# Kernel tuning notes

Measured on AMD Instinct MI355X. Metric: run time of the kernel, lower is better.

The kernel has to match this reference:

```python
import jax, jax.numpy as jnp
import numpy as np

U, G, I, D = 10000, 3000, 8000, 32
LAYERS, SOCIAL_LAYERS = 3, 2
NNZ_UI, NNZ_GI = 720000, 440000
L_MEM = 20
B = 4096


def setup_inputs() -> dict:
    key = jax.random.key(0)
    ks = jax.random.split(key, 24)
    s_u = 1.0 / np.sqrt(U).astype(np.float32)
    s_i = 1.0 / np.sqrt(I).astype(np.float32)
    return {
        "group_inputs": jax.random.randint(ks[0], (B,), 0, G, dtype=jnp.int32),
        "item_inputs": jax.random.randint(ks[1], (B,), 0, I, dtype=jnp.int32),
        "user_emb": jax.random.normal(ks[2], (U, D), jnp.float32) * 0.1,
        "group_emb": jax.random.normal(ks[3], (G, D), jnp.float32) * 0.1,
        "item_emb": jax.random.normal(ks[4], (I, D), jnp.float32) * 0.1,
        "ui_rows": jax.random.randint(ks[5], (NNZ_UI,), 0, U + I, dtype=jnp.int32),
        "ui_cols": jax.random.randint(ks[6], (NNZ_UI,), 0, U + I, dtype=jnp.int32),
        "ui_vals": jax.random.uniform(ks[7], (NNZ_UI,), jnp.float32) * 0.02,
        "gi_rows": jax.random.randint(ks[8], (NNZ_GI,), 0, G + I, dtype=jnp.int32),
        "gi_cols": jax.random.randint(ks[9], (NNZ_GI,), 0, G + I, dtype=jnp.int32),
        "gi_vals": jax.random.uniform(ks[10], (NNZ_GI,), jnp.float32) * 0.02,
        "overlap_user": jax.random.normal(ks[11], (U, U), jnp.float32) * (0.1 * s_u),
        "overlap_item": jax.random.normal(ks[12], (I, I), jnp.float32) * (0.1 * s_i),
        "all_group_users": jax.random.randint(ks[13], (G, L_MEM), 0, U, dtype=jnp.int32),
        "all_group_mask": jax.random.uniform(ks[14], (G, L_MEM), jnp.float32) / L_MEM,
        "gate_w1": jax.random.normal(ks[15], (D, D), jnp.float32) * 0.1,
        "gate_b1": jnp.zeros((D,), jnp.float32),
        "gate_w2": jax.random.normal(ks[16], (D, 1), jnp.float32) * 0.1,
        "gate_b2": jnp.zeros((1,), jnp.float32),
        "pred_w1": jax.random.normal(ks[17], (D, 8), jnp.float32) * 0.1,
        "pred_b1": jnp.zeros((8,), jnp.float32),
        "pred_w2": jax.random.normal(ks[18], (8, 1), jnp.float32) * 0.1,
        "pred_b2": jnp.zeros((1,), jnp.float32),
    }


def _spmm(rows, cols, vals, x, n):
    # COO sparse-dense matmul: out[r] += vals * x[c]
    return jax.ops.segment_sum(vals[:, None] * x[cols], rows, num_segments=n)


def reference(group_inputs, item_inputs, user_emb, group_emb, item_emb,
              ui_rows, ui_cols, ui_vals, gi_rows, gi_cols, gi_vals,
              overlap_user, overlap_item, all_group_users, all_group_mask,
              gate_w1, gate_b1, gate_w2, gate_b2,
              pred_w1, pred_b1, pred_w2, pred_b2):
    # ---- GraphConvolution: user-item propagation ----
    ui = jnp.concatenate([user_emb, item_emb])           # [U+I, D]
    embs_ui = [ui]
    for _ in range(LAYERS):
        ui = _spmm(ui_rows, ui_cols, ui_vals, ui, U + I)
        embs_ui.append(ui)
    user_layers = [e[:U] for e in embs_ui]
    item_layers = [e[U:] for e in embs_ui]
    user_emb_for_user = jnp.mean(jnp.stack(user_layers, 1), axis=1)   # [U, D]
    item_emb_for_user = jnp.mean(jnp.stack(item_layers, 1), axis=1)   # [I, D]

    # ---- group-item propagation ----
    gi = jnp.concatenate([group_emb, item_emb_for_user])  # [G+I, D]
    embs_gi = [gi]
    for _ in range(LAYERS):
        gi = _spmm(gi_rows, gi_cols, gi_vals, gi, G + I)
        embs_gi.append(gi)
    group_gi = [e[:G] for e in embs_gi]
    item_gi = [e[G:] for e in embs_gi]
    i_emb = jnp.mean(jnp.stack(item_gi, 1), axis=1)       # [I, D]

    g_layers = []
    for i in range(LAYERS + 1):
        if i % 2 == 0:
            g_layers.append(group_gi[i])
        else:
            emb_in = jnp.concatenate([group_emb, item_layers[i - 1]])
            g_layers.append(_spmm(gi_rows, gi_cols, gi_vals, emb_in, G + I)[:G])
    g_emb = jnp.mean(jnp.stack(g_layers, 1), axis=1)      # [G, D]

    # ---- SocialRelationshipAgg (dense power-series + gathered pooling) ----
    ue = user_emb_for_user
    acc = ue
    for _ in range(SOCIAL_LAYERS):
        ue = overlap_user @ ue
        acc = acc + ue
    members = acc[all_group_users]                        # [G, L, D]
    group_userlayer = jnp.einsum('gl,gld->gd', all_group_mask, members)

    # ---- Gate ----
    x = jnp.concatenate([g_emb, group_userlayer])         # [2G, D]
    h = jax.nn.relu(x @ gate_w1 + gate_b1)
    w = jax.nn.sigmoid(h @ gate_w2 + gate_b2)             # [2G, 1]
    group_final = w[:G] * g_emb + w[G:] * group_userlayer

    # ---- OverlapGraphConvolution on items ----
    it = i_emb
    iacc = it
    for _ in range(SOCIAL_LAYERS):
        it = overlap_item @ it
        iacc = iacc + it

    # ---- Predict ----
    ge = group_final[group_inputs]                        # [B, D]
    ie = iacc[item_inputs]                                # [B, D]
    p = jax.nn.relu((ge * ie) @ pred_w1 + pred_b1)
    return jax.nn.sigmoid(p @ pred_w2 + pred_b2)          # [B, 1]
```

## Files before the change

### kernel.cpp

```cpp
#include <hip/hip_runtime.h>
#include <math.h>

#define U_N 10000
#define G_N 3000
#define I_N 8000
#define D_N 32
#define NNZ_UI 720000
#define NNZ_GI 440000
#define L_MEM 20
#define B_N 4096
#define UI_N (U_N + I_N)
#define GI_N (G_N + I_N)
#define CAP 128

static __host__ int cdiv(int a, int b) { return (a + b - 1) / b; }

typedef __attribute__((ext_vector_type(8))) short bf16x8;
typedef __attribute__((ext_vector_type(4))) float f32x4;

__device__ __forceinline__ short f32_to_bf16(float f) {
    unsigned u = __float_as_uint(f);
    unsigned r = (u + 0x7FFFu + ((u >> 16) & 1u)) >> 16;
    return (short)r;
}


__global__ __launch_bounds__(256) void bucket_fill2(const int* __restrict__ uir,
                                                    const int* __restrict__ uic,
                                                    const float* __restrict__ uiv,
                                                    const int* __restrict__ gir,
                                                    const int* __restrict__ gic,
                                                    const float* __restrict__ giv,
                                                    int* __restrict__ cnt_ui,
                                                    int* __restrict__ cnt_gi,
                                                    int2* __restrict__ bkt_ui,
                                                    int2* __restrict__ bkt_gi) {
    int i = blockIdx.x * 256 + threadIdx.x;
    if (i < NNZ_UI) {
        int r = uir[i];
        int pos = atomicAdd(&cnt_ui[r], 1);
        if (pos < CAP) {
            int2 e; e.x = uic[i]; e.y = __float_as_int(uiv[i]);
            bkt_ui[(size_t)r * CAP + pos] = e;
        }
        return;
    }
    int k = i - NNZ_UI;
    if (k < NNZ_GI) {
        int r = gir[k];
        int pos = atomicAdd(&cnt_gi[r], 1);
        if (pos < CAP) {
            int2 e; e.x = gic[k]; e.y = __float_as_int(giv[k]);
            bkt_gi[(size_t)r * CAP + pos] = e;
        }
    }
}

#define GATHER(e) ((e.x < split) ? x1[(size_t)e.x * 32 + d] \
                                 : x2[(size_t)(e.x - split) * 32 + d])

__global__ __launch_bounds__(256) void spmm_split(const int* __restrict__ cnt,
                                                  const int2* __restrict__ bkt,
                                                  const float* __restrict__ x1,
                                                  const float* __restrict__ x2,
                                                  int split,
                                                  float* __restrict__ out, int nrows) {
    int row = blockIdx.x * 8 + (threadIdx.x >> 5);
    if (row >= nrows) return;
    int d = threadIdx.x & 31;
    int deg = cnt[row];
    if (deg > CAP) deg = CAP;
    const int2* bk = bkt + (size_t)row * CAP;
    float acc = 0.f;
    int j = 0;
    for (; j + 3 < deg; j += 4) {
        int2 e0 = bk[j], e1 = bk[j + 1], e2 = bk[j + 2], e3 = bk[j + 3];
        float g0 = GATHER(e0), g1 = GATHER(e1), g2 = GATHER(e2), g3 = GATHER(e3);
        acc = fmaf(__int_as_float(e0.y), g0, acc);
        acc = fmaf(__int_as_float(e1.y), g1, acc);
        acc = fmaf(__int_as_float(e2.y), g2, acc);
        acc = fmaf(__int_as_float(e3.y), g3, acc);
    }
    for (; j < deg; ++j) {
        int2 e = bk[j];
        acc = fmaf(__int_as_float(e.y), GATHER(e), acc);
    }
    out[(size_t)row * 32 + d] = acc;
}

__global__ __launch_bounds__(256) void spmm_g2(const int* __restrict__ cnt,
                                               const int2* __restrict__ bkt,
                                               const float* __restrict__ gemb0,
                                               const float* __restrict__ iemb0,
                                               const float* __restrict__ ui2item,
                                               float* __restrict__ gt1,
                                               float* __restrict__ gt3) {
    int row = blockIdx.x * 8 + (threadIdx.x >> 5);
    if (row >= 2 * G_N) return;
    int g = (row < G_N) ? row : row - G_N;
    const float* x1 = gemb0;
    const float* x2 = (row < G_N) ? iemb0 : ui2item;
    const int split = G_N;
    float* out = (row < G_N) ? gt1 : gt3;
    int d = threadIdx.x & 31;
    int deg = cnt[g];
    if (deg > CAP) deg = CAP;
    const int2* bk = bkt + (size_t)g * CAP;
    float acc = 0.f;
    int j = 0;
    for (; j + 3 < deg; j += 4) {
        int2 e0 = bk[j], e1 = bk[j + 1], e2 = bk[j + 2], e3 = bk[j + 3];
        float g0 = GATHER(e0), g1 = GATHER(e1), g2 = GATHER(e2), g3 = GATHER(e3);
        acc = fmaf(__int_as_float(e0.y), g0, acc);
        acc = fmaf(__int_as_float(e1.y), g1, acc);
        acc = fmaf(__int_as_float(e2.y), g2, acc);
        acc = fmaf(__int_as_float(e3.y), g3, acc);
    }
    for (; j < deg; ++j) {
        int2 e = bk[j];
        acc = fmaf(__int_as_float(e.y), GATHER(e), acc);
    }
    out[(size_t)g * 32 + d] = acc;
}
#undef GATHER


__global__ __launch_bounds__(256) void mean_ui(const float* __restrict__ uemb,
                                               const float* __restrict__ iemb0,
                                               const float* __restrict__ ui1,
                                               const float* __restrict__ ui2,
                                               const float* __restrict__ ui3,
                                               float* __restrict__ uefu,
                                               float* __restrict__ accu,
                                               float* __restrict__ iefu) {
    int idx = blockIdx.x * 256 + threadIdx.x;
    if (idx >= UI_N * 32) return;
    const int UOFF = U_N * 32;
    float base = (idx < UOFF) ? uemb[idx] : iemb0[idx - UOFF];
    float m = 0.25f * (base + ui1[idx] + ui2[idx] + ui3[idx]);
    if (idx < UOFF) { uefu[idx] = m; accu[idx] = m; }
    else iefu[idx - UOFF] = m;
}

__global__ __launch_bounds__(256) void mean_gi_items(const float* __restrict__ iefu,
                                                     const float* __restrict__ gi1,
                                                     const float* __restrict__ gi2,
                                                     const float* __restrict__ gi3,
                                                     float* __restrict__ iemb,
                                                     float* __restrict__ iacc) {
    int idx = blockIdx.x * 256 + threadIdx.x;
    if (idx >= I_N * 32) return;
    const int GOFF = G_N * 32;
    float m = 0.25f * (iefu[idx] + gi1[GOFF + idx] + gi2[GOFF + idx] + gi3[GOFF + idx]);
    iemb[idx] = m;
    iacc[idx] = m;
}


__global__ __launch_bounds__(256) void pack_xb(const float* __restrict__ x,
                                               short* __restrict__ XB, int N, int ktiles) {
    int idx = blockIdx.x * 256 + threadIdx.x;
    int total = ktiles * 2 * 64;
    if (idx >= total) return;
    int lane = idx & 63;
    int th = idx >> 6;
    int h = th & 1;
    int t = th >> 1;
    int q = lane >> 4;
    int n = (lane & 15) + h * 16;
    short v[8];
#pragma unroll
    for (int j = 0; j < 8; ++j) {
        int c = t * 32 + q * 8 + j;
        v[j] = (c < N) ? f32_to_bf16(x[(size_t)c * 32 + n]) : (short)0;
    }
    short* dst = XB + (size_t)idx * 8;
#pragma unroll
    for (int j = 0; j < 8; ++j) dst[j] = v[j];
}

__global__ __launch_bounds__(512) void dense_mfma_b(const float* __restrict__ A,
                                                    const short* __restrict__ XB,
                                                    float* __restrict__ out,
                                                    const float* __restrict__ add1,
                                                    int N, int ktiles) {
    __shared__ float red[8 * 512];
    int tid = threadIdx.x;
    int w = tid >> 6;
    int lane = tid & 63;
    int r0 = blockIdx.x << 4;
    int m = lane & 15;
    int q = lane >> 4;
    const float* arow = A + (size_t)(r0 + m) * N + q * 8;
    const bf16x8* xb = (const bf16x8*)XB;
    f32x4 acc0 = {0.f, 0.f, 0.f, 0.f};
    f32x4 acc1 = {0.f, 0.f, 0.f, 0.f};
    for (int t = w; t < ktiles; t += 8) {
        int c0 = t * 32;
        bf16x8 afrag;
        if (c0 + 32 <= N) {
            float4 lo = *(const float4*)(arow + c0);
            float4 hi = *(const float4*)(arow + c0 + 4);
            afrag[0] = f32_to_bf16(lo.x); afrag[1] = f32_to_bf16(lo.y);
            afrag[2] = f32_to_bf16(lo.z); afrag[3] = f32_to_bf16(lo.w);
            afrag[4] = f32_to_bf16(hi.x); afrag[5] = f32_to_bf16(hi.y);
            afrag[6] = f32_to_bf16(hi.z); afrag[7] = f32_to_bf16(hi.w);
        } else {
#pragma unroll
            for (int j = 0; j < 8; ++j) {
                int c = c0 + q * 8 + j;
                afrag[j] = (c < N) ? f32_to_bf16(arow[c0 + j]) : (short)0;
            }
        }
        bf16x8 b0 = xb[(size_t)(t * 2 + 0) * 64 + lane];
        bf16x8 b1 = xb[(size_t)(t * 2 + 1) * 64 + lane];
        acc0 = __builtin_amdgcn_mfma_f32_16x16x32_bf16(afrag, b0, acc0, 0, 0, 0);
        acc1 = __builtin_amdgcn_mfma_f32_16x16x32_bf16(afrag, b1, acc1, 0, 0, 0);
    }
    float* my = red + w * 512;
#pragma unroll
    for (int i = 0; i < 4; ++i) {
        my[(q * 4 + i) * 32 + m]      = acc0[i];
        my[(q * 4 + i) * 32 + m + 16] = acc1[i];
    }
    __syncthreads();
    float s = red[tid];
#pragma unroll
    for (int wv = 1; wv < 8; ++wv) s += red[wv * 512 + tid];
    int row = tid >> 5;
    int col = tid & 31;
    size_t o = (size_t)(r0 + row) * 32 + col;
    out[o] = add1 ? (out[o] + add1[o] + s) : s;
}

__global__ __launch_bounds__(256) void pool_gate_mix(const int* __restrict__ users,
                                                     const float* __restrict__ mask,
                                                     const float* __restrict__ accu,
                                                     const float* __restrict__ gemb0,
                                                     const float* __restrict__ gt1,
                                                     const float* __restrict__ gi2,
                                                     const float* __restrict__ gt3,
                                                     const float* __restrict__ W1,
                                                     const float* __restrict__ b1,
                                                     const float* __restrict__ w2,
                                                     const float* __restrict__ b2,
                                                     float* __restrict__ gfin) {
    int g = blockIdx.x * 8 + (threadIdx.x >> 5);
    if (g >= G_N) return;
    int j = threadIdx.x & 31;
    size_t gj = (size_t)g * 32 + j;
    float ge = 0.25f * (gemb0[gj] + gt1[gj] + gi2[gj] + gt3[gj]);
    float gl = 0.f;
#pragma unroll
    for (int l = 0; l < L_MEM; ++l) {
        int u = users[g * L_MEM + l];
        gl = fmaf(mask[g * L_MEM + l], accu[(size_t)u * 32 + j], gl);
    }
    float h1 = b1[j], h2 = b1[j];
#pragma unroll
    for (int k = 0; k < 32; ++k) {
        float w = W1[k * 32 + j];
        h1 = fmaf(__shfl(ge, k, 32), w, h1);
        h2 = fmaf(__shfl(gl, k, 32), w, h2);
    }
    float w2j = w2[j];
    float t1 = fmaxf(h1, 0.f) * w2j;
    float t2 = fmaxf(h2, 0.f) * w2j;
#pragma unroll
    for (int off = 16; off >= 1; off >>= 1) {
        t1 += __shfl_xor(t1, off, 32);
        t2 += __shfl_xor(t2, off, 32);
    }
    float bb = b2[0];
    float wa = 1.f / (1.f + expf(-(t1 + bb)));
    float wb = 1.f / (1.f + expf(-(t2 + bb)));
    gfin[gj] = wa * ge + wb * gl;
}

__global__ __launch_bounds__(256) void predict_kernel(const int* __restrict__ gidx,
                                                      const int* __restrict__ iidx,
                                                      const float* __restrict__ gfin,
                                                      const float* __restrict__ iacc,
                                                      const float* __restrict__ pw1,
                                                      const float* __restrict__ pb1,
                                                      const float* __restrict__ pw2,
                                                      const float* __restrict__ pb2,
                                                      float* __restrict__ out) {
    int b = blockIdx.x * 256 + threadIdx.x;
    if (b >= B_N) return;
    const float* ge = gfin + (size_t)gidx[b] * 32;
    const float* ie = iacc + (size_t)iidx[b] * 32;
    float p[8];
#pragma unroll
    for (int j = 0; j < 8; ++j) p[j] = pb1[j];
    for (int d = 0; d < 32; ++d) {
        float t = ge[d] * ie[d];
#pragma unroll
        for (int j = 0; j < 8; ++j) p[j] = fmaf(t, pw1[d * 8 + j], p[j]);
    }
    float s = pb2[0];
#pragma unroll
    for (int j = 0; j < 8; ++j) s = fmaf(fmaxf(p[j], 0.f), pw2[j], s);
    out[b] = 1.f / (1.f + expf(-s));
}


extern "C" void kernel_launch(void* const* d_in, const int* in_sizes, int n_in,
                              void* d_out, int out_size, void* d_ws, size_t ws_size,
                              hipStream_t stream) {
    const int*   gin   = (const int*)d_in[0];
    const int*   iin   = (const int*)d_in[1];
    const float* uemb  = (const float*)d_in[2];
    const float* gemb0 = (const float*)d_in[3];
    const float* iemb0 = (const float*)d_in[4];
    const int*   uir   = (const int*)d_in[5];
    const int*   uic   = (const int*)d_in[6];
    const float* uiv   = (const float*)d_in[7];
    const int*   gir   = (const int*)d_in[8];
    const int*   gic   = (const int*)d_in[9];
    const float* giv   = (const float*)d_in[10];
    const float* ov_u  = (const float*)d_in[11];
    const float* ov_i  = (const float*)d_in[12];
    const int*   agu   = (const int*)d_in[13];
    const float* agm   = (const float*)d_in[14];
    const float* gw1   = (const float*)d_in[15];
    const float* gb1   = (const float*)d_in[16];
    const float* gw2   = (const float*)d_in[17];
    const float* gb2   = (const float*)d_in[18];
    const float* pw1   = (const float*)d_in[19];
    const float* pb1   = (const float*)d_in[20];
    const float* pw2   = (const float*)d_in[21];
    const float* pb2   = (const float*)d_in[22];
    float* out = (float*)d_out;

    const int KT_U = (U_N + 31) / 32;
    const int KT_I = I_N / 32;

    char* wp = (char*)d_ws;
    auto alloc = [&](size_t nbytes) -> void* {
        void* p = (void*)wp;
        wp += (nbytes + 255) & ~(size_t)255;
        return p;
    };
    int*   cnt_ui = (int*)alloc((size_t)UI_N * 4);
    int*   cnt_gi = (int*)alloc((size_t)GI_N * 4);
    size_t zbytes = (size_t)(wp - (char*)cnt_ui);

    int2*  bkt_ui = (int2*)alloc((size_t)UI_N * CAP * 8);
    int2*  bkt_gi = (int2*)alloc((size_t)GI_N * CAP * 8);
    float* uea  = (float*)alloc((size_t)U_N * 32 * 4);
    float* ita  = (float*)alloc((size_t)I_N * 32 * 4);
    float* ui1  = (float*)alloc((size_t)UI_N * 32 * 4);
    float* ui2  = (float*)alloc((size_t)UI_N * 32 * 4);
    float* ui3  = (float*)alloc((size_t)UI_N * 32 * 4);
    float* gi1  = (float*)alloc((size_t)GI_N * 32 * 4);
    float* gi2  = (float*)alloc((size_t)GI_N * 32 * 4);
    float* gi3  = (float*)alloc((size_t)GI_N * 32 * 4);
    float* uefu = (float*)alloc((size_t)U_N * 32 * 4);
    float* iefu = (float*)alloc((size_t)I_N * 32 * 4);
    float* iemb = (float*)alloc((size_t)I_N * 32 * 4);
    float* gt1  = (float*)alloc((size_t)G_N * 32 * 4);
    float* gt3  = (float*)alloc((size_t)G_N * 32 * 4);
    float* accu = (float*)alloc((size_t)U_N * 32 * 4);
    float* gfin = (float*)alloc((size_t)G_N * 32 * 4);
    float* iacc = (float*)alloc((size_t)I_N * 32 * 4);
    short* xbu  = (short*)alloc((size_t)KT_U * 2 * 64 * 8 * 2);
    short* xbi  = (short*)alloc((size_t)KT_I * 2 * 64 * 8 * 2);

    (void)hipMemsetAsync(cnt_ui, 0, zbytes, stream);
    bucket_fill2<<<cdiv(NNZ_UI + NNZ_GI, 256), 256, 0, stream>>>(
        uir, uic, uiv, gir, gic, giv, cnt_ui, cnt_gi, bkt_ui, bkt_gi);

    spmm_split<<<cdiv(UI_N, 8), 256, 0, stream>>>(cnt_ui, bkt_ui, uemb, iemb0, U_N, ui1, UI_N);
    spmm_split<<<cdiv(UI_N, 8), 256, 0, stream>>>(cnt_ui, bkt_ui, ui1, ui1 + (size_t)U_N * 32, U_N, ui2, UI_N);
    spmm_split<<<cdiv(UI_N, 8), 256, 0, stream>>>(cnt_ui, bkt_ui, ui2, ui2 + (size_t)U_N * 32, U_N, ui3, UI_N);
    spmm_g2<<<cdiv(2 * G_N, 8), 256, 0, stream>>>(cnt_gi, bkt_gi, gemb0, iemb0,
                                                  ui2 + (size_t)U_N * 32, gt1, gt3);
    mean_ui<<<cdiv(UI_N * 32, 256), 256, 0, stream>>>(uemb, iemb0, ui1, ui2, ui3, uefu, accu, iefu);

    spmm_split<<<cdiv(GI_N, 8), 256, 0, stream>>>(cnt_gi, bkt_gi, gemb0, iefu, G_N, gi1, GI_N);
    spmm_split<<<cdiv(GI_N, 8), 256, 0, stream>>>(cnt_gi, bkt_gi, gi1, gi1 + (size_t)G_N * 32, G_N, gi2, GI_N);
    spmm_split<<<cdiv(GI_N, 8), 256, 0, stream>>>(cnt_gi, bkt_gi, gi2, gi2 + (size_t)G_N * 32, G_N, gi3, GI_N);
    mean_gi_items<<<cdiv(I_N * 32, 256), 256, 0, stream>>>(iefu, gi1, gi2, gi3, iemb, iacc);

    const int U_STRIPS = U_N / 16, I_STRIPS = I_N / 16;
    pack_xb<<<cdiv(KT_U * 128, 256), 256, 0, stream>>>(uefu, xbu, U_N, KT_U);
    dense_mfma_b<<<U_STRIPS, 512, 0, stream>>>(ov_u, xbu, uea, nullptr, U_N, KT_U);
    pack_xb<<<cdiv(KT_U * 128, 256), 256, 0, stream>>>(uea, xbu, U_N, KT_U);
    dense_mfma_b<<<U_STRIPS, 512, 0, stream>>>(ov_u, xbu, accu, uea, U_N, KT_U);

    pool_gate_mix<<<cdiv(G_N, 8), 256, 0, stream>>>(agu, agm, accu, gemb0, gt1, gi2, gt3,
                                                    gw1, gb1, gw2, gb2, gfin);

    pack_xb<<<cdiv(KT_I * 128, 256), 256, 0, stream>>>(iemb, xbi, I_N, KT_I);
    dense_mfma_b<<<I_STRIPS, 512, 0, stream>>>(ov_i, xbi, ita, nullptr, I_N, KT_I);
    pack_xb<<<cdiv(KT_I * 128, 256), 256, 0, stream>>>(ita, xbi, I_N, KT_I);
    dense_mfma_b<<<I_STRIPS, 512, 0, stream>>>(ov_i, xbi, iacc, ita, I_N, KT_I);

    predict_kernel<<<cdiv(B_N, 256), 256, 0, stream>>>(gin, iin, gfin, iacc,
                                                       pw1, pb1, pw2, pb2, out);
}
```

Baseline: 1.106 ms.

## Compute final item overlap layer only for queried items and trim GI spmm

Marks the unique item indices used by the prediction batch and builds a compact row list. The last dense overlap-item matmul now runs only over those rows, instead of all 8000, reading only the needed rows of the large overlap matrix. The third group-item spmm layer skips group rows, whose results are not consumed. It adds a small marking kernel and an atomic-built row list. Rows of iacc for unqueried items are left incomplete.

```diff
diff --git a/kernel.cpp b/kernel.cpp
--- a/kernel.cpp
+++ b/kernel.cpp
@@ -56,6 +56,20 @@
     }
 }
 
+__global__ __launch_bounds__(256) void mark_items(const int* __restrict__ iidx,
+                                                  int* __restrict__ iflags,
+                                                  int* __restrict__ icount,
+                                                  int* __restrict__ ilist) {
+    int b = blockIdx.x * 256 + threadIdx.x;
+    if (b >= B_N) return;
+    int it = iidx[b];
+    if (it < 0 || it >= I_N) return;
+    if (atomicExch(&iflags[it], 1) == 0) {
+        int p = atomicAdd(icount, 1);
+        if (p < B_N) ilist[p] = it;
+    }
+}
+
 #define GATHER(e) ((e.x < split) ? x1[(size_t)e.x * 32 + d] \
                                  : x2[(size_t)(e.x - split) * 32 + d])
 
@@ -64,8 +78,9 @@
                                                   const float* __restrict__ x1,
                                                   const float* __restrict__ x2,
                                                   int split,
-                                                  float* __restrict__ out, int nrows) {
-    int row = blockIdx.x * 8 + (threadIdx.x >> 5);
+                                                  float* __restrict__ out,
+                                                  int row0, int nrows) {
+    int row = row0 + blockIdx.x * 8 + (threadIdx.x >> 5);
     if (row >= nrows) return;
     int d = threadIdx.x & 31;
     int deg = cnt[row];
@@ -233,6 +248,68 @@
     out[o] = add1 ? (out[o] + add1[o] + s) : s;
 }
 
+__global__ __launch_bounds__(512) void dense_mfma_trim(const float* __restrict__ A,
+                                                       const short* __restrict__ XB,
+                                                       float* __restrict__ out,
+                                                       const float* __restrict__ add1,
+                                                       const int* __restrict__ rowlist,
+                                                       const int* __restrict__ rowcount,
+                                                       int N, int ktiles) {
+    __shared__ float red[8 * 512];
+    int cnt = *rowcount;
+    if (cnt < 1) return;
+    if (cnt > B_N) cnt = B_N;
+    int r0 = blockIdx.x << 4;
+    if (r0 >= cnt) return;
+    int tid = threadIdx.x;
+    int w = tid >> 6;
+    int lane = tid & 63;
+    int m = lane & 15;
+    int q = lane >> 4;
+    int ci = r0 + m;
+    if (ci >= cnt) ci = cnt - 1;
+    int arow_g = rowlist[ci];
+    if (arow_g < 0 || arow_g >= I_N) arow_g = 0;
+    const float* arow = A + (size_t)arow_g * N + q * 8;
+    const bf16x8* xb = (const bf16x8*)XB;
+    f32x4 acc0 = {0.f, 0.f, 0.f, 0.f};
+    f32x4 acc1 = {0.f, 0.f, 0.f, 0.f};
+    for (int t = w; t < ktiles; t += 8) {
+        int c0 = t * 32;
+        float4 lo = *(const float4*)(arow + c0);
+        float4 hi = *(const float4*)(arow + c0 + 4);
+        bf16x8 afrag;
+        afrag[0] = f32_to_bf16(lo.x); afrag[1] = f32_to_bf16(lo.y);
+        afrag[2] = f32_to_bf16(lo.z); afrag[3] = f32_to_bf16(lo.w);
+        afrag[4] = f32_to_bf16(hi.x); afrag[5] = f32_to_bf16(hi.y);
+        afrag[6] = f32_to_bf16(hi.z); afrag[7] = f32_to_bf16(hi.w);
+        bf16x8 b0 = xb[(size_t)(t * 2 + 0) * 64 + lane];
+        bf16x8 b1 = xb[(size_t)(t * 2 + 1) * 64 + lane];
+        acc0 = __builtin_amdgcn_mfma_f32_16x16x32_bf16(afrag, b0, acc0, 0, 0, 0);
+        acc1 = __builtin_amdgcn_mfma_f32_16x16x32_bf16(afrag, b1, acc1, 0, 0, 0);
+    }
+    float* my = red + w * 512;
+#pragma unroll
+    for (int i = 0; i < 4; ++i) {
+        my[(q * 4 + i) * 32 + m]      = acc0[i];
+        my[(q * 4 + i) * 32 + m + 16] = acc1[i];
+    }
+    __syncthreads();
+    float s = red[tid];
+#pragma unroll
+    for (int wv = 1; wv < 8; ++wv) s += red[wv * 512 + tid];
+    int row = tid >> 5;
+    int col = tid & 31;
+    int gidx = r0 + row;
+    if (gidx < cnt) {
+        int orow = rowlist[gidx];
+        if (orow >= 0 && orow < I_N) {
+            size_t o = (size_t)orow * 32 + col;
+            out[o] = out[o] + add1[o] + s;
+        }
+    }
+}
+
 __global__ __launch_bounds__(256) void pool_gate_mix(const int* __restrict__ users,
                                                      const float* __restrict__ mask,
                                                      const float* __restrict__ accu,
@@ -344,7 +421,10 @@
     };
     int*   cnt_ui = (int*)alloc((size_t)UI_N * 4);
     int*   cnt_gi = (int*)alloc((size_t)GI_N * 4);
+    int*   iflags = (int*)alloc((size_t)I_N * 4);
+    int*   icount = (int*)alloc(4);
     size_t zbytes = (size_t)(wp - (char*)cnt_ui);
+    int*   ilist  = (int*)alloc((size_t)B_N * 4);
 
     int2*  bkt_ui = (int2*)alloc((size_t)UI_N * CAP * 8);
     int2*  bkt_gi = (int2*)alloc((size_t)GI_N * CAP * 8);
@@ -370,17 +450,18 @@
     (void)hipMemsetAsync(cnt_ui, 0, zbytes, stream);
     bucket_fill2<<<cdiv(NNZ_UI + NNZ_GI, 256), 256, 0, stream>>>(
         uir, uic, uiv, gir, gic, giv, cnt_ui, cnt_gi, bkt_ui, bkt_gi);
-
-    spmm_split<<<cdiv(UI_N, 8), 256, 0, stream>>>(cnt_ui, bkt_ui, uemb, iemb0, U_N, ui1, UI_N);
-    spmm_split<<<cdiv(UI_N, 8), 256, 0, stream>>>(cnt_ui, bkt_ui, ui1, ui1 + (size_t)U_N * 32, U_N, ui2, UI_N);
-    spmm_split<<<cdiv(UI_N, 8), 256, 0, stream>>>(cnt_ui, bkt_ui, ui2, ui2 + (size_t)U_N * 32, U_N, ui3, UI_N);
+    mark_items<<<cdiv(B_N, 256), 256, 0, stream>>>(iin, iflags, icount, ilist);
+
+    spmm_split<<<cdiv(UI_N, 8), 256, 0, stream>>>(cnt_ui, bkt_ui, uemb, iemb0, U_N, ui1, 0, UI_N);
+    spmm_split<<<cdiv(UI_N, 8), 256, 0, stream>>>(cnt_ui, bkt_ui, ui1, ui1 + (size_t)U_N * 32, U_N, ui2, 0, UI_N);
+    spmm_split<<<cdiv(UI_N, 8), 256, 0, stream>>>(cnt_ui, bkt_ui, ui2, ui2 + (size_t)U_N * 32, U_N, ui3, 0, UI_N);
     spmm_g2<<<cdiv(2 * G_N, 8), 256, 0, stream>>>(cnt_gi, bkt_gi, gemb0, iemb0,
                                                   ui2 + (size_t)U_N * 32, gt1, gt3);
     mean_ui<<<cdiv(UI_N * 32, 256), 256, 0, stream>>>(uemb, iemb0, ui1, ui2, ui3, uefu, accu, iefu);
 
-    spmm_split<<<cdiv(GI_N, 8), 256, 0, stream>>>(cnt_gi, bkt_gi, gemb0, iefu, G_N, gi1, GI_N);
-    spmm_split<<<cdiv(GI_N, 8), 256, 0, stream>>>(cnt_gi, bkt_gi, gi1, gi1 + (size_t)G_N * 32, G_N, gi2, GI_N);
-    spmm_split<<<cdiv(GI_N, 8), 256, 0, stream>>>(cnt_gi, bkt_gi, gi2, gi2 + (size_t)G_N * 32, G_N, gi3, GI_N);
+    spmm_split<<<cdiv(GI_N, 8), 256, 0, stream>>>(cnt_gi, bkt_gi, gemb0, iefu, G_N, gi1, 0, GI_N);
+    spmm_split<<<cdiv(GI_N, 8), 256, 0, stream>>>(cnt_gi, bkt_gi, gi1, gi1 + (size_t)G_N * 32, G_N, gi2, 0, GI_N);
+    spmm_split<<<cdiv(I_N, 8), 256, 0, stream>>>(cnt_gi, bkt_gi, gi2, gi2 + (size_t)G_N * 32, G_N, gi3, G_N, GI_N);
     mean_gi_items<<<cdiv(I_N * 32, 256), 256, 0, stream>>>(iefu, gi1, gi2, gi3, iemb, iacc);
 
     const int U_STRIPS = U_N / 16, I_STRIPS = I_N / 16;
@@ -395,7 +476,7 @@
     pack_xb<<<cdiv(KT_I * 128, 256), 256, 0, stream>>>(iemb, xbi, I_N, KT_I);
     dense_mfma_b<<<I_STRIPS, 512, 0, stream>>>(ov_i, xbi, ita, nullptr, I_N, KT_I);
     pack_xb<<<cdiv(KT_I * 128, 256), 256, 0, stream>>>(ita, xbi, I_N, KT_I);
-    dense_mfma_b<<<I_STRIPS, 512, 0, stream>>>(ov_i, xbi, iacc, ita, I_N, KT_I);
+    dense_mfma_trim<<<cdiv(B_N, 16), 512, 0, stream>>>(ov_i, xbi, iacc, ita, ilist, icount, I_N, KT_I);
 
     predict_kernel<<<cdiv(B_N, 256), 256, 0, stream>>>(gin, iin, gfin, iacc,
                                                        pw1, pb1, pw2, pb2, out);
```

Result: faster. 1.081 ms (-2.3%).
